# Kernel optimization log

Hardware: AMD Instinct MI355X
Metric: run time of the kernel (lower is better)

## Reference

```python
import jax, jax.numpy as jnp
import numpy as np

# dims
B, S, T = 64, 128, 64            # batch, src_len, tgt_len
H, E, V = 1024, 512, 16000       # hidden, embedding, vocab
ENC = 2 * H                      # bidirectional encoder dim
SOS = 1
SCALE = 0.02


def setup_inputs() -> dict:
    key = jax.random.key(0)
    ks = jax.random.split(key, 13)
    n = lambda k, sh: jax.random.normal(k, sh, dtype=jnp.float32) * SCALE
    return {
        "encoder_outputs": jax.random.normal(ks[0], (B, S, ENC), dtype=jnp.float32),
        "encoder_hidden": jax.random.normal(ks[1], (1, B, H), dtype=jnp.float32),
        "target": jax.random.randint(ks[2], (B, T), 0, V, dtype=jnp.int64),
        "emb": n(ks[3], (V, E)),                 # embedding table
        "Wa": n(ks[4], (H, H + ENC)),            # attn Linear weight ([query | enc] -> H)
        "ba": jnp.zeros((H,), jnp.float32),
        "v": n(ks[5], (H,)),                     # attn score vector (no bias)
        "W_ih": n(ks[6], (3 * H, E + ENC)),      # GRU input weights (r,z,n)
        "b_ih": jnp.zeros((3 * H,), jnp.float32),
        "W_hh": n(ks[7], (3 * H, H)),            # GRU hidden weights
        "b_hh": jnp.zeros((3 * H,), jnp.float32),
        "Wo": n(ks[8], (V, H)),                  # output projection
        "bo": jnp.zeros((V,), jnp.float32),
    }


def reference(encoder_outputs, encoder_hidden, target, emb, Wa, ba, v,
              W_ih, b_ih, W_hh, b_hh, Wo, bo):
    h0 = encoder_hidden[0]                                   # [B,H] (num_layers=1)
    # teacher_forcing_p=1.0 -> decoder input is SOS then target[:, :-1]
    tokens = jnp.concatenate(
        [jnp.full((B, 1), SOS, dtype=target.dtype), target[:, :-1]], axis=1)  # [B,T]

    # attn Linear acts on concat([query, enc_out]); split weight accordingly
    Wa_q, Wa_e = Wa[:, :H], Wa[:, H:]
    # encoder part is time-invariant -> precompute once: [B,S,H]
    enc_proj = jnp.einsum('bse,he->bsh', encoder_outputs, Wa_e)

    def step(h, tok):
        x_emb = emb[tok]                                     # [B,E]
        q = h @ Wa_q.T + ba                                  # [B,H]
        energy = jnp.tanh(q[:, None, :] + enc_proj)          # [B,S,H]
        scores = energy @ v                                  # [B,S]
        alpha = jax.nn.softmax(scores, axis=1)               # [B,S]
        ctx = jnp.einsum('bs,bsd->bd', alpha, encoder_outputs)  # [B,ENC]
        x = jnp.concatenate([x_emb, ctx], axis=1)            # [B,E+ENC]
        # torch GRU cell
        gi = x @ W_ih.T + b_ih                               # [B,3H]
        gh = h @ W_hh.T + b_hh
        ir, iz, inn = jnp.split(gi, 3, axis=1)
        hr, hz, hn = jnp.split(gh, 3, axis=1)
        r = jax.nn.sigmoid(ir + hr)
        z = jax.nn.sigmoid(iz + hz)
        n = jnp.tanh(inn + r * hn)
        h_new = (1.0 - z) * n + z * h                        # [B,H]
        out = h_new @ Wo.T + bo                              # [B,V]
        return h_new, out

    _, outs = jax.lax.scan(step, h0, tokens.T)               # [T,B,V]
    return jnp.transpose(outs, (1, 0, 2))                    # [B,T,V]
```

## Files before the change

kernel.cpp:

```cpp
#include <hip/hip_runtime.h>
#include <hip/hip_bf16.h>

#define B_   64
#define S_   128
#define T_   64
#define H_   1024
#define E_   512
#define V_   16000
#define ENC_ 2048
#define XDIM_ (E_ + ENC_)
#define G3_  (3 * H_)
#define QGH_ (4 * H_)
#define NB_  256

#define SMEM_ENCP   0
#define SMEM_SCR    65536
#define SMEM_TOTAL  102400

typedef __attribute__((ext_vector_type(8))) short bf16x8;
typedef __attribute__((ext_vector_type(8))) unsigned short u16x8;
typedef __attribute__((ext_vector_type(4))) float f32x4;

__device__ __forceinline__ ushort f2bf(float x) {
    __hip_bfloat16 h = __float2bfloat16(x);
    return *reinterpret_cast<ushort*>(&h);
}
__device__ __forceinline__ float bf2f(ushort u) {
    return __uint_as_float((unsigned)u << 16);
}
__device__ __forceinline__ float sigmoidf_(float x) {
    return 1.f / (1.f + expf(-x));
}

template <typename T>
__device__ __forceinline__ void atstore(T* p, T v) {
    __hip_atomic_store(p, v, __ATOMIC_RELAXED, __HIP_MEMORY_SCOPE_AGENT);
}

__device__ __forceinline__ void gload_lds16(const ushort* g, ushort* l) {
    __builtin_amdgcn_global_load_lds(
        (const __attribute__((address_space(1))) unsigned int*)g,
        (__attribute__((address_space(3))) unsigned int*)l, 16, 0, 0);
}

__device__ __forceinline__ void pollge(const unsigned* f, unsigned v) {
    while (__hip_atomic_load(f, __ATOMIC_RELAXED, __HIP_MEMORY_SCOPE_AGENT) < v)
        __builtin_amdgcn_s_sleep(1);
}
__device__ __forceinline__ void sigrel(unsigned* f, unsigned v) {
    __hip_atomic_store(f, v, __ATOMIC_RELAXED, __HIP_MEMORY_SCOPE_AGENT);
}

__device__ __forceinline__ void gbar(unsigned* flags, unsigned* go, unsigned gen) {
    __syncthreads();
    const int tid = threadIdx.x;
    if (blockIdx.x == 0) {
        if (tid >= 1 && tid < NB_) pollge(&flags[tid * 32], gen);
        __syncthreads();
        if (tid < 32) sigrel(&go[tid * 32], gen);
    } else {
        if (tid == 0) {
            sigrel(&flags[blockIdx.x * 32], gen);
            pollge(&go[(blockIdx.x >> 3) * 32], gen);
        }
    }
    __syncthreads();
}

__global__ __launch_bounds__(256) void gemm128_bf16(
    const ushort* __restrict__ A, int lda,
    const ushort* __restrict__ W, int ldw,
    const float* __restrict__ bias,
    float* __restrict__ Cf, ushort* __restrict__ Cb, int ldc,
    int K)
{
    const int bn0 = blockIdx.x * 128;
    const int bm0 = blockIdx.y * 128;
    const int tid = threadIdx.x;
    const int wv  = tid >> 6;
    const int lane = tid & 63;

    __shared__ ushort As[128 * 32];
    __shared__ ushort Bs[128 * 32];

    const int srow = tid >> 2;
    const int scol = (tid & 3) * 8;

    const ushort* gA0 = A + (size_t)(bm0 + srow) * lda + scol;
    const ushort* gA1 = gA0 + (size_t)64 * lda;
    const ushort* gB0 = W + (size_t)(bn0 + srow) * ldw + scol;
    const ushort* gB1 = gB0 + (size_t)64 * ldw;

    ushort* lA0 = &As[tid * 8];
    ushort* lA1 = &As[2048 + tid * 8];
    ushort* lB0 = &Bs[tid * 8];
    ushort* lB1 = &Bs[2048 + tid * 8];

    const int wr0 = (wv >> 1) * 64;
    const int wc0 = (wv & 1) * 64;
    const int frow = lane & 15;
    const int fk   = (lane >> 4) * 8;

    f32x4 acc[4][4];
#pragma unroll
    for (int i = 0; i < 4; ++i)
#pragma unroll
        for (int j = 0; j < 4; ++j) acc[i][j] = (f32x4){0.f, 0.f, 0.f, 0.f};

    for (int k0 = 0; k0 < K; k0 += 32) {
        gload_lds16(gA0 + k0, lA0);
        gload_lds16(gA1 + k0, lA1);
        gload_lds16(gB0 + k0, lB0);
        gload_lds16(gB1 + k0, lB1);
        __syncthreads();

        bf16x8 af[4], bf[4];
#pragma unroll
        for (int rb = 0; rb < 4; ++rb)
            af[rb] = *reinterpret_cast<const bf16x8*>(&As[(wr0 + rb * 16 + frow) * 32 + fk]);
#pragma unroll
        for (int cb = 0; cb < 4; ++cb)
            bf[cb] = *reinterpret_cast<const bf16x8*>(&Bs[(wc0 + cb * 16 + frow) * 32 + fk]);
#pragma unroll
        for (int rb = 0; rb < 4; ++rb)
#pragma unroll
            for (int cb = 0; cb < 4; ++cb)
                acc[rb][cb] = __builtin_amdgcn_mfma_f32_16x16x32_bf16(af[rb], bf[cb], acc[rb][cb], 0, 0, 0);
        __syncthreads();
    }

    const int quad = lane >> 4;
#pragma unroll
    for (int cb = 0; cb < 4; ++cb) {
        const int col = bn0 + wc0 + cb * 16 + frow;
        const float bv = bias ? bias[col] : 0.f;
#pragma unroll
        for (int rb = 0; rb < 4; ++rb) {
            const int row0 = bm0 + wr0 + rb * 16 + quad * 4;
            f32x4 a = acc[rb][cb];
#pragma unroll
            for (int r = 0; r < 4; ++r) {
                const float val = a[r] + bv;
                if (Cb) Cb[(size_t)(row0 + r) * ldc + col] = f2bf(val);
                else    Cf[(size_t)(row0 + r) * ldc + col] = val;
            }
        }
    }
}

__global__ __launch_bounds__(256) void pack_bf16(
    const float* __restrict__ src, int src_ld, int c0, int ncols,
    ushort* __restrict__ dst, size_t total)
{
    size_t i = (size_t)blockIdx.x * 256 + threadIdx.x;
    const size_t stride = (size_t)gridDim.x * 256;
    for (; i < total; i += stride) {
        size_t r = i / (size_t)ncols;
        int c = (int)(i - r * (size_t)ncols);
        dst[i] = f2bf(src[r * (size_t)src_ld + c0 + c]);
    }
}

__global__ __launch_bounds__(256) void gather_emb(
    const int* __restrict__ target, const float* __restrict__ emb,
    ushort* __restrict__ dst)
{
    const int row = blockIdx.x;
    const int b = row >> 6;
    const int t = row & 63;
    const int tok = (t == 0) ? 1 : target[b * T_ + t - 1];
    const float* e = emb + (size_t)tok * E_;
    ushort* d = dst + (size_t)row * E_;
    for (int c = threadIdx.x; c < E_; c += 256) d[c] = f2bf(e[c]);
}

__global__ __launch_bounds__(256) void pack_bhq(
    const float* __restrict__ ba, const float* __restrict__ bhh,
    float* __restrict__ dst)
{
    const int j = blockIdx.x * 256 + threadIdx.x;
    if (j < H_) dst[j] = ba[j];
    else if (j < QGH_) dst[j] = bhh[j - H_];
}

__global__ __launch_bounds__(256) void barinit(unsigned* f) {
    const int i = blockIdx.x * 256 + threadIdx.x;
    if (i < 17408) f[i] = 0u;
}

__global__ __launch_bounds__(512) void decoder_persist(
    const ushort* __restrict__ encp,
    const ushort* __restrict__ enc,
    const ushort* __restrict__ ench,
    const float*  __restrict__ ench_f,
    const ushort* __restrict__ Whq,
    const ushort* __restrict__ Wie,
    const float*  __restrict__ bhq,
    const float*  __restrict__ vvec,
    const float*  __restrict__ giemb,
    float* __restrict__ q_all,
    float* __restrict__ scores_all,
    ushort* __restrict__ ctx_all,
    float* __restrict__ hall_f,
    ushort* __restrict__ hall_b,
    unsigned* __restrict__ flags,
    unsigned* __restrict__ go,
    unsigned* __restrict__ sflag)
{
    extern __shared__ __align__(16) char smem[];
    const int blk = blockIdx.x;
    const int tid = threadIdx.x;
    const int wv = tid >> 6;
    const int lane = tid & 63;
    const int frow = lane & 15;
    const int fk = (lane >> 4) * 8;

    const int ab = blk >> 2;
    const int aq = blk & 3;
    const int qbg = blk >> 6;
    const int qc0 = (blk & 63) * 16;
    const int jt = blk >> 2;
    const int cb0 = (blk & 3) * 16;

    {
        const char* src = (const char*)(encp + ((size_t)ab * S_ + aq * 32) * H_);
#pragma unroll
        for (int r = 0; r < 8; ++r) {
            const int ci = r * 8 + wv;
            gload_lds16((const ushort*)(src + ci * 1024 + lane * 16),
                        (ushort*)(smem + SMEM_ENCP + ci * 1024 + lane * 16));
        }
    }
    float vr[16];
    *reinterpret_cast<f32x4*>(&vr[0])  = *reinterpret_cast<const f32x4*>(vvec + lane * 8);
    *reinterpret_cast<f32x4*>(&vr[4])  = *reinterpret_cast<const f32x4*>(vvec + lane * 8 + 4);
    *reinterpret_cast<f32x4*>(&vr[8])  = *reinterpret_cast<const f32x4*>(vvec + 512 + lane * 8);
    *reinterpret_cast<f32x4*>(&vr[12]) = *reinterpret_cast<const f32x4*>(vvec + 512 + lane * 8 + 4);
    __syncthreads();

    unsigned gen = 0;

    for (int t = 0; t < T_; ++t) {
        const ushort* hb = t ? (hall_b + (size_t)(t - 1) * H_) : ench;
        const float*  hf = t ? (hall_f + (size_t)(t - 1) * H_) : ench_f;
        const int ldh = t ? (T_ * H_) : H_;
        float* q = q_all + (size_t)t * B_ * H_;
        float* scores = scores_all + (size_t)t * B_ * S_;
        ushort* ctx = ctx_all + (size_t)t * B_ * ENC_;

        {
            f32x4 (*red)[64] = reinterpret_cast<f32x4(*)[64]>(smem + SMEM_SCR);
            const ushort* Arow = hb + (size_t)(qbg * 16 + frow) * ldh + wv * 128 + fk;
            const ushort* Brow = Whq + (size_t)(qc0 + frow) * H_ + wv * 128 + fk;
            f32x4 acc = (f32x4){0.f, 0.f, 0.f, 0.f};
#pragma unroll
            for (int c = 0; c < 4; ++c) {
                bf16x8 a = *reinterpret_cast<const bf16x8*>(Arow + c * 32);
                bf16x8 b = *reinterpret_cast<const bf16x8*>(Brow + c * 32);
                acc = __builtin_amdgcn_mfma_f32_16x16x32_bf16(a, b, acc, 0, 0, 0);
            }
            red[wv][lane] = acc;
            __syncthreads();
            if (wv == 0) {
                f32x4 s = red[0][lane];
#pragma unroll
                for (int w = 1; w < 8; ++w) s += red[w][lane];
                const int col = qc0 + frow;
                const float bv = bhq[col];
                const int b0 = qbg * 16 + (lane >> 4) * 4;
#pragma unroll
                for (int r = 0; r < 4; ++r)
                    atstore(&q[(size_t)(b0 + r) * H_ + col], s[r] + bv);
            }
        }
        gbar(flags, go, ++gen);

        {
            float qr[16];
            const float* qrow = q + (size_t)ab * H_;
            *reinterpret_cast<f32x4*>(&qr[0])  = *reinterpret_cast<const f32x4*>(qrow + lane * 8);
            *reinterpret_cast<f32x4*>(&qr[4])  = *reinterpret_cast<const f32x4*>(qrow + lane * 8 + 4);
            *reinterpret_cast<f32x4*>(&qr[8])  = *reinterpret_cast<const f32x4*>(qrow + 512 + lane * 8);
            *reinterpret_cast<f32x4*>(&qr[12]) = *reinterpret_cast<const f32x4*>(qrow + 512 + lane * 8 + 4);
#pragma unroll
            for (int i = 0; i < 4; ++i) {
                const int sl = wv * 4 + i;
                const char* rowp = smem + SMEM_ENCP + sl * 2048;
                u16x8 e0 = *reinterpret_cast<const u16x8*>(rowp + lane * 16);
                u16x8 e1 = *reinterpret_cast<const u16x8*>(rowp + 1024 + lane * 16);
                float p = 0.f;
#pragma unroll
                for (int j = 0; j < 8; ++j)
                    p += vr[j] * tanhf(qr[j] + bf2f(e0[j]));
#pragma unroll
                for (int j = 0; j < 8; ++j)
                    p += vr[8 + j] * tanhf(qr[8 + j] + bf2f(e1[j]));
#pragma unroll
                for (int off = 32; off; off >>= 1) p += __shfl_xor(p, off);
                if (lane == 0) atstore(&scores[ab * S_ + aq * 32 + sl], p);
            }
            __syncthreads();
            if (tid == 0) sigrel(&sflag[blk * 32], (unsigned)(t + 1));

            const int e0c = aq * 512;
            const ushort* ebase = enc + (size_t)ab * S_ * ENC_ + e0c + lane * 8;
            u16x8 epre[16];
#pragma unroll
            for (int i = 0; i < 16; ++i)
                epre[i] = *reinterpret_cast<const u16x8*>(ebase + (size_t)(wv + i * 8) * ENC_);

            if (tid < 4) pollge(&sflag[(ab * 4 + tid) * 32], (unsigned)(t + 1));
            __syncthreads();

            float* part = reinterpret_cast<float*>(smem + SMEM_SCR);
            float* al   = reinterpret_cast<float*>(smem + SMEM_SCR + 16384);
            if (tid < 64) {
                float a0 = scores[ab * S_ + tid];
                float a1 = scores[ab * S_ + tid + 64];
                float m = fmaxf(a0, a1);
#pragma unroll
                for (int off = 32; off; off >>= 1) m = fmaxf(m, __shfl_xor(m, off));
                float e0v = expf(a0 - m), e1v = expf(a1 - m);
                float ssum = e0v + e1v;
#pragma unroll
                for (int off = 32; off; off >>= 1) ssum += __shfl_xor(ssum, off);
                const float inv = 1.f / ssum;
                al[tid] = e0v * inv;
                al[tid + 64] = e1v * inv;
            }
            __syncthreads();
            float acc[8];
#pragma unroll
            for (int j = 0; j < 8; ++j) acc[j] = 0.f;
#pragma unroll
            for (int i = 0; i < 16; ++i) {
                u16x8 ev = epre[i];
                const float a = al[wv + i * 8];
#pragma unroll
                for (int j = 0; j < 8; ++j)
                    acc[j] = fmaf(a, bf2f(ev[j]), acc[j]);
            }
            *reinterpret_cast<f32x4*>(part + wv * 512 + lane * 8)     = *reinterpret_cast<f32x4*>(&acc[0]);
            *reinterpret_cast<f32x4*>(part + wv * 512 + lane * 8 + 4) = *reinterpret_cast<f32x4*>(&acc[4]);
            __syncthreads();
            float scol = part[tid];
#pragma unroll
            for (int w = 1; w < 8; ++w) scol += part[w * 512 + tid];
            atstore(&ctx[(size_t)ab * ENC_ + e0c + tid], f2bf(scol));
        }
        gbar(flags, go, ++gen);

        {
            f32x4 (*redp)[4][64] = reinterpret_cast<f32x4(*)[4][64]>(smem + SMEM_SCR);
            float (*gt)[16][16] = reinterpret_cast<float(*)[16][16]>(smem + SMEM_SCR + 32768);
            const int j0 = jt * 16;

            f32x4 a0 = (f32x4){0.f, 0.f, 0.f, 0.f};
            f32x4 a1 = a0;
            f32x4 a2 = a0;
            f32x4 a3 = a0;

            {
                const ushort* Ar = hb + (size_t)(cb0 + frow) * ldh + wv * 128 + fk;
                const ushort* Br = Whq + (size_t)(1024 + j0 + frow) * H_ + wv * 128 + fk;
                const ushort* Bz = Br + (size_t)1024 * H_;
                const ushort* Bn = Br + (size_t)2048 * H_;
#pragma unroll
                for (int c = 0; c < 4; ++c) {
                    bf16x8 av = *reinterpret_cast<const bf16x8*>(Ar + c * 32);
                    a0 = __builtin_amdgcn_mfma_f32_16x16x32_bf16(av, *reinterpret_cast<const bf16x8*>(Br + c * 32), a0, 0, 0, 0);
                    a1 = __builtin_amdgcn_mfma_f32_16x16x32_bf16(av, *reinterpret_cast<const bf16x8*>(Bz + c * 32), a1, 0, 0, 0);
                    a3 = __builtin_amdgcn_mfma_f32_16x16x32_bf16(av, *reinterpret_cast<const bf16x8*>(Bn + c * 32), a3, 0, 0, 0);
                }
            }
            {
                const ushort* Ar = ctx + (size_t)(cb0 + frow) * ENC_ + wv * 256 + fk;
                const ushort* Br = Wie + (size_t)(j0 + frow) * ENC_ + wv * 256 + fk;
                const ushort* Bz = Br + (size_t)1024 * ENC_;
                const ushort* Bn = Br + (size_t)2048 * ENC_;
#pragma unroll
                for (int c = 0; c < 8; ++c) {
                    bf16x8 av = *reinterpret_cast<const bf16x8*>(Ar + c * 32);
                    a0 = __builtin_amdgcn_mfma_f32_16x16x32_bf16(av, *reinterpret_cast<const bf16x8*>(Br + c * 32), a0, 0, 0, 0);
                    a1 = __builtin_amdgcn_mfma_f32_16x16x32_bf16(av, *reinterpret_cast<const bf16x8*>(Bz + c * 32), a1, 0, 0, 0);
                    a2 = __builtin_amdgcn_mfma_f32_16x16x32_bf16(av, *reinterpret_cast<const bf16x8*>(Bn + c * 32), a2, 0, 0, 0);
                }
            }
            redp[wv][0][lane] = a0;
            redp[wv][1][lane] = a1;
            redp[wv][2][lane] = a2;
            redp[wv][3][lane] = a3;
            __syncthreads();
            if (wv < 4) {
                f32x4 s = redp[0][wv][lane];
#pragma unroll
                for (int w = 1; w < 8; ++w) s += redp[w][wv][lane];
                const int row0 = (lane >> 4) * 4;
#pragma unroll
                for (int r = 0; r < 4; ++r) gt[wv][row0 + r][frow] = s[r];
            }
            __syncthreads();
            if (tid < 256) {
                const int bl = tid >> 4, jl = tid & 15;
                const int b = cb0 + bl;
                const int j = j0 + jl;
                const size_t gr = (size_t)(b * T_ + t) * G3_;
                const float rsum = gt[0][bl][jl] + giemb[gr + j]          + bhq[1024 + j];
                const float zsum = gt[1][bl][jl] + giemb[gr + H_ + j]     + bhq[2048 + j];
                const float inn  = gt[2][bl][jl] + giemb[gr + 2 * H_ + j];
                const float hn   = gt[3][bl][jl] + bhq[3072 + j];
                const float r = sigmoidf_(rsum);
                const float z = sigmoidf_(zsum);
                const float n = tanhf(inn + r * hn);
                const float hnew = (1.f - z) * n + z * hf[(size_t)b * ldh + j];
                const size_t ho = (size_t)b * (T_ * H_) + (size_t)t * H_ + j;
                atstore(&hall_f[ho], hnew);
                atstore(&hall_b[ho], f2bf(hnew));
            }
        }
        gbar(flags, go, ++gen);
    }
}

static inline int pgrid(size_t total) {
    size_t nb = (total + 255) / 256;
    if (nb > 4096) nb = 4096;
    return (int)nb;
}

extern "C" void kernel_launch(void* const* d_in, const int* in_sizes, int n_in,
                              void* d_out, int out_size, void* d_ws, size_t ws_size,
                              hipStream_t stream) {
    const float* enc    = (const float*)d_in[0];
    const float* enc_h  = (const float*)d_in[1];
    const int*   target = (const int*)  d_in[2];
    const float* emb    = (const float*)d_in[3];
    const float* Wa     = (const float*)d_in[4];
    const float* ba     = (const float*)d_in[5];
    const float* vvec   = (const float*)d_in[6];
    const float* W_ih   = (const float*)d_in[7];
    const float* b_ih   = (const float*)d_in[8];
    const float* W_hh   = (const float*)d_in[9];
    const float* b_hh   = (const float*)d_in[10];
    const float* Wo     = (const float*)d_in[11];
    const float* bo     = (const float*)d_in[12];
    float* out = (float*)d_out;

    char* p = (char*)d_ws;
    auto alloc_u16 = [&](size_t n) { ushort* r = (ushort*)p; p += n * 2; return r; };
    auto alloc_f32 = [&](size_t n) { float* r = (float*)p; p += n * 4; return r; };

    ushort* enc_bf  = alloc_u16((size_t)B_ * S_ * ENC_);
    ushort* encp_bf = alloc_u16((size_t)B_ * S_ * H_);
    ushort* Wo_bf   = alloc_u16((size_t)V_ * H_);
    ushort* Wae_bf  = alloc_u16((size_t)H_ * ENC_);
    ushort* Whq_bf  = alloc_u16((size_t)QGH_ * H_);
    ushort* Wie_bf  = alloc_u16((size_t)G3_ * ENC_);
    ushort* Wiee_bf = alloc_u16((size_t)G3_ * E_);
    ushort* ench_bf = alloc_u16((size_t)B_ * H_);
    ushort* Xemb_bf = alloc_u16((size_t)B_ * T_ * E_);
    ushort* hall_bf = alloc_u16((size_t)B_ * T_ * H_);
    ushort* ctx_all = alloc_u16((size_t)T_ * B_ * ENC_);
    float* hall_f   = alloc_f32((size_t)B_ * T_ * H_);
    float* giemb    = alloc_f32((size_t)B_ * T_ * G3_);
    float* q_all    = alloc_f32((size_t)T_ * B_ * H_);
    float* scr_all  = alloc_f32((size_t)T_ * B_ * S_);
    float* bhq      = alloc_f32((size_t)QGH_);
    unsigned* flags = (unsigned*)alloc_f32(17664);
    unsigned* go    = flags + 8192;
    unsigned* sflag = flags + 9216;

    const int LDW = H_ + ENC_;

    pack_bf16<<<pgrid((size_t)B_*S_*ENC_), 256, 0, stream>>>(enc, ENC_, 0, ENC_, enc_bf, (size_t)B_*S_*ENC_);
    pack_bf16<<<pgrid((size_t)V_*H_), 256, 0, stream>>>(Wo, H_, 0, H_, Wo_bf, (size_t)V_*H_);
    pack_bf16<<<pgrid((size_t)H_*ENC_), 256, 0, stream>>>(Wa, LDW, H_, ENC_, Wae_bf, (size_t)H_*ENC_);
    pack_bf16<<<pgrid((size_t)H_*H_), 256, 0, stream>>>(Wa, LDW, 0, H_, Whq_bf, (size_t)H_*H_);
    pack_bf16<<<pgrid((size_t)G3_*H_), 256, 0, stream>>>(W_hh, H_, 0, H_, Whq_bf + (size_t)H_*H_, (size_t)G3_*H_);
    pack_bf16<<<pgrid((size_t)G3_*ENC_), 256, 0, stream>>>(W_ih, XDIM_, E_, ENC_, Wie_bf, (size_t)G3_*ENC_);
    pack_bf16<<<pgrid((size_t)G3_*E_), 256, 0, stream>>>(W_ih, XDIM_, 0, E_, Wiee_bf, (size_t)G3_*E_);
    pack_bf16<<<pgrid((size_t)B_*H_), 256, 0, stream>>>(enc_h, H_, 0, H_, ench_bf, (size_t)B_*H_);
    gather_emb<<<B_*T_, 256, 0, stream>>>(target, emb, Xemb_bf);
    pack_bhq<<<QGH_/256, 256, 0, stream>>>(ba, b_hh, bhq);
    barinit<<<69, 256, 0, stream>>>(flags);

    gemm128_bf16<<<dim3(H_/128, (B_*S_)/128), 256, 0, stream>>>(
        enc_bf, ENC_, Wae_bf, ENC_, nullptr, nullptr, encp_bf, H_, ENC_);
    gemm128_bf16<<<dim3(G3_/128, (B_*T_)/128), 256, 0, stream>>>(
        Xemb_bf, E_, Wiee_bf, E_, b_ih, giemb, nullptr, G3_, E_);

    decoder_persist<<<NB_, 512, SMEM_TOTAL, stream>>>(
        encp_bf, enc_bf, ench_bf, enc_h, Whq_bf, Wie_bf, bhq, vvec, giemb,
        q_all, scr_all, ctx_all, hall_f, hall_bf, flags, go, sflag);

    gemm128_bf16<<<dim3(V_/128, (B_*T_)/128), 256, 0, stream>>>(
        hall_bf, H_, Wo_bf, H_, bo, out, nullptr, V_, H_);
}
```

Baseline: 2.937 ms.

## Replace global barriers with per-stage producer/consumer dataflow flags

Replaces the three grid-wide barriers per decoder step with targeted flag signalling. Each block publishes a per-stage flag, and consumers poll only the 64 producer blocks whose outputs they actually read (q rows, ctx columns, h rows). The aim is to cut barrier latency and let blocks run ahead independently. The cost is more flag memory and polling traffic, plus a correctness risk if a dependency set is wrong or if relaxed atomics give insufficient memory ordering.

```diff
diff --git a/kernel.cpp b/kernel.cpp
--- a/kernel.cpp
+++ b/kernel.cpp
@@ -49,22 +49,6 @@
 }
 __device__ __forceinline__ void sigrel(unsigned* f, unsigned v) {
     __hip_atomic_store(f, v, __ATOMIC_RELAXED, __HIP_MEMORY_SCOPE_AGENT);
-}
-
-__device__ __forceinline__ void gbar(unsigned* flags, unsigned* go, unsigned gen) {
-    __syncthreads();
-    const int tid = threadIdx.x;
-    if (blockIdx.x == 0) {
-        if (tid >= 1 && tid < NB_) pollge(&flags[tid * 32], gen);
-        __syncthreads();
-        if (tid < 32) sigrel(&go[tid * 32], gen);
-    } else {
-        if (tid == 0) {
-            sigrel(&flags[blockIdx.x * 32], gen);
-            pollge(&go[(blockIdx.x >> 3) * 32], gen);
-        }
-    }
-    __syncthreads();
 }
 
 __global__ __launch_bounds__(256) void gemm128_bf16(
@@ -185,7 +169,7 @@
 
 __global__ __launch_bounds__(256) void barinit(unsigned* f) {
     const int i = blockIdx.x * 256 + threadIdx.x;
-    if (i < 17408) f[i] = 0u;
+    if (i < 32768) f[i] = 0u;
 }
 
 __global__ __launch_bounds__(512) void decoder_persist(
@@ -203,9 +187,10 @@
     ushort* __restrict__ ctx_all,
     float* __restrict__ hall_f,
     ushort* __restrict__ hall_b,
-    unsigned* __restrict__ flags,
-    unsigned* __restrict__ go,
-    unsigned* __restrict__ sflag)
+    unsigned* __restrict__ aflag,
+    unsigned* __restrict__ sflag,
+    unsigned* __restrict__ xflag,
+    unsigned* __restrict__ hflag)
 {
     extern __shared__ __align__(16) char smem[];
     const int blk = blockIdx.x;
@@ -238,8 +223,6 @@
     *reinterpret_cast<f32x4*>(&vr[12]) = *reinterpret_cast<const f32x4*>(vvec + 512 + lane * 8 + 4);
     __syncthreads();
 
-    unsigned gen = 0;
-
     for (int t = 0; t < T_; ++t) {
         const ushort* hb = t ? (hall_b + (size_t)(t - 1) * H_) : ench;
         const float*  hf = t ? (hall_f + (size_t)(t - 1) * H_) : ench_f;
@@ -248,6 +231,11 @@
         float* scores = scores_all + (size_t)t * B_ * S_;
         ushort* ctx = ctx_all + (size_t)t * B_ * ENC_;
 
+        if (t) {
+            if (tid < 64) pollge(&hflag[(tid * 4 + qbg) * 32], (unsigned)t);
+            __syncthreads();
+        }
+
         {
             f32x4 (*red)[64] = reinterpret_cast<f32x4(*)[64]>(smem + SMEM_SCR);
             const ushort* Arow = hb + (size_t)(qbg * 16 + frow) * ldh + wv * 128 + fk;
@@ -273,7 +261,11 @@
                     atstore(&q[(size_t)(b0 + r) * H_ + col], s[r] + bv);
             }
         }
-        gbar(flags, go, ++gen);
+        __syncthreads();
+        if (tid == 0) sigrel(&aflag[blk * 32], (unsigned)(t + 1));
+
+        if (tid < 64) pollge(&aflag[((ab >> 4) * 64 + tid) * 32], (unsigned)(t + 1));
+        __syncthreads();
 
         {
             float qr[16];
@@ -348,7 +340,11 @@
             for (int w = 1; w < 8; ++w) scol += part[w * 512 + tid];
             atstore(&ctx[(size_t)ab * ENC_ + e0c + tid], f2bf(scol));
         }
-        gbar(flags, go, ++gen);
+        __syncthreads();
+        if (tid == 0) sigrel(&xflag[blk * 32], (unsigned)(t + 1));
+
+        if (tid < 64) pollge(&xflag[(cb0 * 4 + tid) * 32], (unsigned)(t + 1));
+        __syncthreads();
 
         {
             f32x4 (*redp)[4][64] = reinterpret_cast<f32x4(*)[4][64]>(smem + SMEM_SCR);
@@ -418,7 +414,8 @@
                 atstore(&hall_b[ho], f2bf(hnew));
             }
         }
-        gbar(flags, go, ++gen);
+        __syncthreads();
+        if (tid == 0) sigrel(&hflag[blk * 32], (unsigned)(t + 1));
     }
 }
 
@@ -466,9 +463,11 @@
     float* q_all    = alloc_f32((size_t)T_ * B_ * H_);
     float* scr_all  = alloc_f32((size_t)T_ * B_ * S_);
     float* bhq      = alloc_f32((size_t)QGH_);
-    unsigned* flags = (unsigned*)alloc_f32(17664);
-    unsigned* go    = flags + 8192;
-    unsigned* sflag = flags + 9216;
+    unsigned* flags = (unsigned*)alloc_f32(33024);
+    unsigned* aflag = flags;
+    unsigned* sflag = flags + 8192;
+    unsigned* xflag = flags + 16384;
+    unsigned* hflag = flags + 24576;
 
     const int LDW = H_ + ENC_;
 
@@ -482,7 +481,7 @@
     pack_bf16<<<pgrid((size_t)B_*H_), 256, 0, stream>>>(enc_h, H_, 0, H_, ench_bf, (size_t)B_*H_);
     gather_emb<<<B_*T_, 256, 0, stream>>>(target, emb, Xemb_bf);
     pack_bhq<<<QGH_/256, 256, 0, stream>>>(ba, b_hh, bhq);
-    barinit<<<69, 256, 0, stream>>>(flags);
+    barinit<<<128, 256, 0, stream>>>(flags);
 
     gemm128_bf16<<<dim3(H_/128, (B_*S_)/128), 256, 0, stream>>>(
         enc_bf, ENC_, Wae_bf, ENC_, nullptr, nullptr, encp_bf, H_, ENC_);
@@ -491,7 +490,7 @@
 
     decoder_persist<<<NB_, 512, SMEM_TOTAL, stream>>>(
         encp_bf, enc_bf, ench_bf, enc_h, Whq_bf, Wie_bf, bhq, vvec, giemb,
-        q_all, scr_all, ctx_all, hall_f, hall_bf, flags, go, sflag);
+        q_all, scr_all, ctx_all, hall_f, hall_bf, aflag, sflag, xflag, hflag);
 
     gemm128_bf16<<<dim3(V_/128, (B_*T_)/128), 256, 0, stream>>>(
         hall_bf, H_, Wo_bf, H_, bo, out, nullptr, V_, H_);
```

Result: faster. 2.834 ms (-3.5%).
